# Kernel tuning notes

Hardware: AMD Instinct MI355X
Metric: run time of the kernel (lower is better)

Reference implementation:

```python
import jax, jax.numpy as jnp
import numpy as np

N, L, S, D, K, H, G = 512, 1024, 3, 128, 4, 32, 64


def setup_inputs() -> dict:
    key = jax.random.key(0)
    ks = jax.random.split(key, 12)
    f = lambda i, shape, s=1.0: jax.random.normal(ks[i], shape, dtype=jnp.float32) * s
    return dict(
        scores=f(0, (N, 1, L, S)),
        veh_repr=f(1, (N, 1, D)),
        cust_repr=f(2, (N, L, D)),
        edge_emb=f(3, (N, 1, L, D)),
        expert_w1=f(4, (K, S, H), 0.3),
        expert_b1=jnp.zeros((K, H), jnp.float32),
        expert_w2=f(5, (K, H, 1), 0.3),
        expert_b2=jnp.zeros((K, 1), jnp.float32),
        sit_w1=f(6, (2 * D, G), 0.05),
        sit_b1=jnp.zeros((G,), jnp.float32),
        sit_w2=f(7, (G, K), 0.1),
        sit_b2=jnp.zeros((K,), jnp.float32),
        cand_w=f(8, (S, K), 0.3),
        cand_b=jnp.zeros((K,), jnp.float32),
        edge_w=f(9, (D, K), 0.05),
        gate_balance=jnp.zeros((), jnp.float32),
    )


def reference(scores, veh_repr, cust_repr, edge_emb,
              expert_w1, expert_b1, expert_w2, expert_b2,
              sit_w1, sit_b1, sit_w2, sit_b2,
              cand_w, cand_b, edge_w, gate_balance):
    # Inference mode: no gate noise, no dropout (identity at eval).
    # Situation gating: vehicle repr + graph context -> (N,1,K) logits
    graph_ctx = cust_repr.mean(axis=1, keepdims=True)              # (N,1,D)
    sit_in = jnp.concatenate([veh_repr, graph_ctx], axis=-1)       # (N,1,2D)
    hg = jax.nn.gelu(sit_in @ sit_w1 + sit_b1, approximate=False)  # (N,1,G)
    sit_logits = hg @ sit_w2 + sit_b2                              # (N,1,K)

    # Candidate-level gating from raw scores + edge embeddings
    cand_logits = scores @ cand_w + cand_b + edge_emb @ edge_w     # (N,1,L,K)

    alpha = jax.nn.sigmoid(gate_balance)
    gate_logits = alpha * sit_logits[:, :, None, :] + (1.0 - alpha) * cand_logits
    gate_w = jax.nn.softmax(gate_logits, axis=-1)                  # (N,1,L,K)

    # Per-expert tiny MLP over the S score channels
    h = jax.nn.gelu(jnp.einsum('nqls,ksh->nqlkh', scores, expert_w1) + expert_b1,
                    approximate=False)                             # (N,1,L,K,H)
    expert_out = jnp.einsum('nqlkh,kho->nqlko', h, expert_w2)[..., 0] + expert_b2[:, 0]

    fused = (gate_w * expert_out).sum(axis=-1)                     # (N,1,L)
    return fused
```

## Files before the change

kernel.cpp:

```cpp
#include <hip/hip_runtime.h>

#define NN 512
#define LL 1024
#define SS 3
#define DD 128
#define KK 4
#define HH 32
#define GG 64

#define DPP_XOR1 0xB1
#define DPP_XOR2 0x4E
#define DPP_ROR4 0x124
#define DPP_ROR8 0x128
#define SWZ16 0x401F

template <int CTRL>
__device__ __forceinline__ float dppf(float x) {
    return __int_as_float(__builtin_amdgcn_update_dpp(
        0, __float_as_int(x), CTRL, 0xF, 0xF, true));
}
__device__ __forceinline__ float swz16f(float x) {
    return __int_as_float(__builtin_amdgcn_ds_swizzle(__float_as_int(x), SWZ16));
}

__device__ __forceinline__ float fast_gelu(float x) {
    const float c0 = 0.7978845608028654f;
    const float c1 = 0.7978845608028654f * 0.044715f;
    float u = x * x;
    float y = x * fmaf(c1, u, c0);
    float e = __expf(2.0f * y);
    float r = __builtin_amdgcn_rcpf(e + 1.0f);
    float t = fmaf(-2.0f, r, 1.0f);
    return 0.5f * x * (1.0f + t);
}

__global__ __launch_bounds__(512, 4) void k_all(
    const float* __restrict__ scores, const float* __restrict__ veh,
    const float* __restrict__ cust, const float* __restrict__ edge,
    const float* __restrict__ ew1, const float* __restrict__ eb1,
    const float* __restrict__ ew2, const float* __restrict__ eb2,
    const float* __restrict__ sw1, const float* __restrict__ sb1,
    const float* __restrict__ sw2, const float* __restrict__ sb2,
    const float* __restrict__ cand_w, const float* __restrict__ cand_b,
    const float* __restrict__ edge_w, const float* __restrict__ gbp,
    float* __restrict__ out)
{
    __shared__ float4 red[512];
    __shared__ float sin_[2 * DD];
    __shared__ float hg[GG];
    __shared__ float slds[KK];
    __shared__ float4 sc4[(LL * SS) / 4];

    const int n = blockIdx.x;
    const int t = threadIdx.x;
    const int lane = t & 63;
    const int r = lane & 31;

    const int ko = r & 3;
    const int jg = r >> 2;
    const bool kb0 = (r & 1) != 0;
    const bool kb1 = (r & 2) != 0;

    {
        const float4* sp4 = (const float4*)(scores + (size_t)n * LL * SS);
        sc4[t] = sp4[t];
        if (t < 256) sc4[512 + t] = sp4[512 + t];
    }

    const float4* ew4 = (const float4*)edge_w;
    const float4 wqa = ew4[4 * r + 0];
    const float4 wqb = ew4[4 * r + 1];
    const float4 wqc = ew4[4 * r + 2];
    const float4 wqd = ew4[4 * r + 3];
    const float cw0 = cand_w[0 * KK + ko];
    const float cw1 = cand_w[1 * KK + ko];
    const float cw2 = cand_w[2 * KK + ko];
    const float cb  = cand_b[ko];
    const float4* w1f = (const float4*)ew1;
    const float4 w1a = w1f[(ko * SS + 0) * (HH / 4) + jg];
    const float4 w1b = w1f[(ko * SS + 1) * (HH / 4) + jg];
    const float4 w1c = w1f[(ko * SS + 2) * (HH / 4) + jg];
    const float4 b1v = ((const float4*)eb1)[ko * (HH / 4) + jg];
    const float4 w2v = ((const float4*)ew2)[ko * (HH / 4) + jg];
    const float b2o8 = 0.125f * eb2[ko];
    const float gbv = gbp[0];
    const float alpha = 1.0f / (1.0f + __expf(-gbv));
    const float onema = 1.0f - alpha;

    const int c = t & 31;
    const int rs = t >> 5;
    const float4* cp = (const float4*)(cust + (size_t)n * LL * DD);
    float4 a0 = make_float4(0.f, 0.f, 0.f, 0.f), a1 = a0, a2 = a0, a3 = a0;
    #pragma unroll 4
    for (int i = 0; i < 16; ++i) {
        float4 v0 = cp[(rs + 16 * i      ) * 32 + c];
        float4 v1 = cp[(rs + 16 * i + 256) * 32 + c];
        float4 v2 = cp[(rs + 16 * i + 512) * 32 + c];
        float4 v3 = cp[(rs + 16 * i + 768) * 32 + c];
        a0.x += v0.x; a0.y += v0.y; a0.z += v0.z; a0.w += v0.w;
        a1.x += v1.x; a1.y += v1.y; a1.z += v1.z; a1.w += v1.w;
        a2.x += v2.x; a2.y += v2.y; a2.z += v2.z; a2.w += v2.w;
        a3.x += v3.x; a3.y += v3.y; a3.z += v3.z; a3.w += v3.w;
    }
    a0.x += a1.x + a2.x + a3.x;
    a0.y += a1.y + a2.y + a3.y;
    a0.z += a1.z + a2.z + a3.z;
    a0.w += a1.w + a2.w + a3.w;
    red[t] = a0;
    __syncthreads();

    if (t < 32) {
        float4 s = red[t];
        #pragma unroll
        for (int i = 1; i < 16; i++) {
            float4 v = red[i * 32 + t];
            s.x += v.x; s.y += v.y; s.z += v.z; s.w += v.w;
        }
        const float inv = 1.0f / (float)LL;
        sin_[DD + 4 * t + 0] = s.x * inv;
        sin_[DD + 4 * t + 1] = s.y * inv;
        sin_[DD + 4 * t + 2] = s.z * inv;
        sin_[DD + 4 * t + 3] = s.w * inv;
        float4 vv = ((const float4*)(veh + (size_t)n * DD))[t];
        sin_[4 * t + 0] = vv.x; sin_[4 * t + 1] = vv.y;
        sin_[4 * t + 2] = vv.z; sin_[4 * t + 3] = vv.w;
    }
    __syncthreads();

    float* redf = (float*)red;
    if (t < 256) {
        const int g = t & 63;
        const int part = t >> 6;
        float a = 0.f;
        #pragma unroll 8
        for (int i = 0; i < 64; ++i) {
            const int row = part * 64 + i;
            a = fmaf(sin_[row], sw1[row * GG + g], a);
        }
        redf[t] = a;
    }
    __syncthreads();
    if (t < GG) {
        float a = sb1[t] + redf[t] + redf[t + 64] + redf[t + 128] + redf[t + 192];
        hg[t] = fast_gelu(a);
    }
    __syncthreads();
    if (t < KK) {
        float a = sb2[t];
        #pragma unroll
        for (int g = 0; g < GG; g++)
            a = fmaf(hg[g], sw2[g * KK + t], a);
        slds[t] = a;
    }
    __syncthreads();

    const float sl0 = slds[0], sl1 = slds[1], sl2 = slds[2], sl3 = slds[3];
    float sa_ = kb0 ? sl1 : sl0;
    float sb_ = kb0 ? sl3 : sl2;
    float so  = kb1 ? sb_ : sa_;
    const float sbase = fmaf(alpha, so, onema * cb);

    const int base_el = t >> 5;
    const float* sc_lds = (const float*)sc4;
    const float* ed_base = edge + (size_t)n * LL * DD;
    float* out_base = out + (size_t)n * LL;

    for (int i = 0; i < 16; ++i) {
        const int e0 = base_el + i * 64;
        float4 ev[4];
        float s0[4], s1[4], s2[4];
        #pragma unroll
        for (int u = 0; u < 4; ++u)
            ev[u] = *(const float4*)(ed_base + (size_t)(e0 + u * 16) * DD + r * 4);
        #pragma unroll
        for (int u = 0; u < 4; ++u) {
            const int el = e0 + u * 16;
            s0[u] = sc_lds[el * 3 + 0];
            s1[u] = sc_lds[el * 3 + 1];
            s2[u] = sc_lds[el * 3 + 2];
        }

        float p0[4], p1[4], p2[4], p3[4];
        #pragma unroll
        for (int u = 0; u < 4; ++u) {
            p0[u] = fmaf(ev[u].x, wqa.x, fmaf(ev[u].y, wqb.x, fmaf(ev[u].z, wqc.x, ev[u].w * wqd.x)));
            p1[u] = fmaf(ev[u].x, wqa.y, fmaf(ev[u].y, wqb.y, fmaf(ev[u].z, wqc.y, ev[u].w * wqd.y)));
            p2[u] = fmaf(ev[u].x, wqa.z, fmaf(ev[u].y, wqb.z, fmaf(ev[u].z, wqc.z, ev[u].w * wqd.z)));
            p3[u] = fmaf(ev[u].x, wqa.w, fmaf(ev[u].y, wqb.w, fmaf(ev[u].z, wqc.w, ev[u].w * wqd.w)));
        }
        float P0[4], P2[4];
        #pragma unroll
        for (int u = 0; u < 4; ++u) {
            float g0 = kb0 ? p0[u] : p1[u];
            float g2 = kb0 ? p2[u] : p3[u];
            float k0 = kb0 ? p1[u] : p0[u];
            float k2 = kb0 ? p3[u] : p2[u];
            P0[u] = k0 + dppf<DPP_XOR1>(g0);
            P2[u] = k2 + dppf<DPP_XOR1>(g2);
        }
        float q[4];
        #pragma unroll
        for (int u = 0; u < 4; ++u) {
            float gv = kb1 ? P0[u] : P2[u];
            float kv = kb1 ? P2[u] : P0[u];
            q[u] = kv + dppf<DPP_XOR2>(gv);
        }
        #pragma unroll
        for (int u = 0; u < 4; ++u) q[u] += dppf<DPP_ROR4>(q[u]);
        #pragma unroll
        for (int u = 0; u < 4; ++u) q[u] += dppf<DPP_ROR8>(q[u]);
        #pragma unroll
        for (int u = 0; u < 4; ++u) q[u] += swz16f(q[u]);

        float ex[4];
        #pragma unroll
        for (int u = 0; u < 4; ++u) {
            float sdot = fmaf(s0[u], cw0, fmaf(s1[u], cw1, s2[u] * cw2));
            float gl = fmaf(onema, sdot + q[u], sbase);
            ex[u] = __expf(gl);
        }
        float se[4];
        #pragma unroll
        for (int u = 0; u < 4; ++u) se[u] = ex[u] + dppf<DPP_XOR1>(ex[u]);
        #pragma unroll
        for (int u = 0; u < 4; ++u) se[u] += dppf<DPP_XOR2>(se[u]);

        float tk[4];
        #pragma unroll
        for (int u = 0; u < 4; ++u) {
            float gw = ex[u] * __builtin_amdgcn_rcpf(se[u]);
            float z, h, acc;
            z = fmaf(s0[u], w1a.x, fmaf(s1[u], w1b.x, fmaf(s2[u], w1c.x, b1v.x))); h = fast_gelu(z); acc = h * w2v.x;
            z = fmaf(s0[u], w1a.y, fmaf(s1[u], w1b.y, fmaf(s2[u], w1c.y, b1v.y))); h = fast_gelu(z); acc = fmaf(h, w2v.y, acc);
            z = fmaf(s0[u], w1a.z, fmaf(s1[u], w1b.z, fmaf(s2[u], w1c.z, b1v.z))); h = fast_gelu(z); acc = fmaf(h, w2v.z, acc);
            z = fmaf(s0[u], w1a.w, fmaf(s1[u], w1b.w, fmaf(s2[u], w1c.w, b1v.w))); h = fast_gelu(z); acc = fmaf(h, w2v.w, acc);
            tk[u] = gw * (acc + b2o8);
        }
        #pragma unroll
        for (int u = 0; u < 4; ++u) tk[u] += dppf<DPP_XOR1>(tk[u]);
        #pragma unroll
        for (int u = 0; u < 4; ++u) tk[u] += dppf<DPP_XOR2>(tk[u]);
        #pragma unroll
        for (int u = 0; u < 4; ++u) tk[u] += dppf<DPP_ROR4>(tk[u]);
        #pragma unroll
        for (int u = 0; u < 4; ++u) tk[u] += dppf<DPP_ROR8>(tk[u]);
        #pragma unroll
        for (int u = 0; u < 4; ++u) tk[u] += swz16f(tk[u]);

        if (r == 0) {
            #pragma unroll
            for (int u = 0; u < 4; ++u)
                out_base[e0 + u * 16] = tk[u];
        }
    }
}

extern "C" void kernel_launch(void* const* d_in, const int* in_sizes, int n_in,
                              void* d_out, int out_size, void* d_ws, size_t ws_size,
                              hipStream_t stream)
{
    const float* scores = (const float*)d_in[0];
    const float* veh    = (const float*)d_in[1];
    const float* cust   = (const float*)d_in[2];
    const float* edge   = (const float*)d_in[3];
    const float* ew1    = (const float*)d_in[4];
    const float* eb1    = (const float*)d_in[5];
    const float* ew2    = (const float*)d_in[6];
    const float* eb2    = (const float*)d_in[7];
    const float* sw1    = (const float*)d_in[8];
    const float* sb1    = (const float*)d_in[9];
    const float* sw2    = (const float*)d_in[10];
    const float* sb2    = (const float*)d_in[11];
    const float* cw     = (const float*)d_in[12];
    const float* cb     = (const float*)d_in[13];
    const float* egw    = (const float*)d_in[14];
    const float* gb     = (const float*)d_in[15];
    float* out = (float*)d_out;

    hipLaunchKernelGGL(k_all, dim3(NN), dim3(512), 0, stream,
                       scores, veh, cust, edge, ew1, eb1, ew2, eb2,
                       sw1, sb1, sw2, sb2, cw, cb, egw, gb, out);
}
```

Baseline: 552.9 us.

## Fuse candidate gating into mean reduction via factored softmax with LDS staging

Moves the per-candidate edge-projection, expert MLP and exp computation into the same loop that sums cust_repr for the graph mean, so both large input streams are read in one pass. The softmax is factored into exp(alpha*situation logit) times exp(candidate logit), so the candidate-dependent part no longer waits for the situation MLP. Per-expert numerators and exponentials are staged in a 32 KB shared buffer and combined in a short final pass. This adds LDS pressure that may reduce occupancy, and drops the per-element softmax normalisation, which is less robust to large logits.

```diff
diff --git a/kernel.cpp b/kernel.cpp
--- a/kernel.cpp
+++ b/kernel.cpp
@@ -50,6 +50,7 @@
     __shared__ float hg[GG];
     __shared__ float slds[KK];
     __shared__ float4 sc4[(LL * SS) / 4];
+    __shared__ float elds[LL * 8];
 
     const int n = blockIdx.x;
     const int t = threadIdx.x;
@@ -86,22 +87,110 @@
     const float gbv = gbp[0];
     const float alpha = 1.0f / (1.0f + __expf(-gbv));
     const float onema = 1.0f - alpha;
+    const float cbase = onema * cb;
+
+    __syncthreads();
 
     const int c = t & 31;
     const int rs = t >> 5;
     const float4* cp = (const float4*)(cust + (size_t)n * LL * DD);
+    const int base_el = t >> 5;
+    const float* sc_lds = (const float*)sc4;
+    const float* ed_base = edge + (size_t)n * LL * DD;
+
     float4 a0 = make_float4(0.f, 0.f, 0.f, 0.f), a1 = a0, a2 = a0, a3 = a0;
-    #pragma unroll 4
+
     for (int i = 0; i < 16; ++i) {
+        const int e0 = base_el + i * 64;
+
+        float4 ev[4];
+        #pragma unroll
+        for (int u = 0; u < 4; ++u)
+            ev[u] = *(const float4*)(ed_base + (size_t)(e0 + u * 16) * DD + r * 4);
         float4 v0 = cp[(rs + 16 * i      ) * 32 + c];
         float4 v1 = cp[(rs + 16 * i + 256) * 32 + c];
         float4 v2 = cp[(rs + 16 * i + 512) * 32 + c];
         float4 v3 = cp[(rs + 16 * i + 768) * 32 + c];
+
+        float s0[4], s1[4], s2[4];
+        #pragma unroll
+        for (int u = 0; u < 4; ++u) {
+            const int el = e0 + u * 16;
+            s0[u] = sc_lds[el * 3 + 0];
+            s1[u] = sc_lds[el * 3 + 1];
+            s2[u] = sc_lds[el * 3 + 2];
+        }
+
+        float p0[4], p1[4], p2[4], p3[4];
+        #pragma unroll
+        for (int u = 0; u < 4; ++u) {
+            p0[u] = fmaf(ev[u].x, wqa.x, fmaf(ev[u].y, wqb.x, fmaf(ev[u].z, wqc.x, ev[u].w * wqd.x)));
+            p1[u] = fmaf(ev[u].x, wqa.y, fmaf(ev[u].y, wqb.y, fmaf(ev[u].z, wqc.y, ev[u].w * wqd.y)));
+            p2[u] = fmaf(ev[u].x, wqa.z, fmaf(ev[u].y, wqb.z, fmaf(ev[u].z, wqc.z, ev[u].w * wqd.z)));
+            p3[u] = fmaf(ev[u].x, wqa.w, fmaf(ev[u].y, wqb.w, fmaf(ev[u].z, wqc.w, ev[u].w * wqd.w)));
+        }
+        float P0[4], P2[4];
+        #pragma unroll
+        for (int u = 0; u < 4; ++u) {
+            float g0 = kb0 ? p0[u] : p1[u];
+            float g2 = kb0 ? p2[u] : p3[u];
+            float k0 = kb0 ? p1[u] : p0[u];
+            float k2 = kb0 ? p3[u] : p2[u];
+            P0[u] = k0 + dppf<DPP_XOR1>(g0);
+            P2[u] = k2 + dppf<DPP_XOR1>(g2);
+        }
+        float q[4];
+        #pragma unroll
+        for (int u = 0; u < 4; ++u) {
+            float gv = kb1 ? P0[u] : P2[u];
+            float kv = kb1 ? P2[u] : P0[u];
+            q[u] = kv + dppf<DPP_XOR2>(gv);
+        }
+        #pragma unroll
+        for (int u = 0; u < 4; ++u) q[u] += dppf<DPP_ROR4>(q[u]);
+        #pragma unroll
+        for (int u = 0; u < 4; ++u) q[u] += dppf<DPP_ROR8>(q[u]);
+        #pragma unroll
+        for (int u = 0; u < 4; ++u) q[u] += swz16f(q[u]);
+
+        float exc[4];
+        #pragma unroll
+        for (int u = 0; u < 4; ++u) {
+            float sdot = fmaf(s0[u], cw0, fmaf(s1[u], cw1, s2[u] * cw2));
+            exc[u] = __expf(fmaf(onema, sdot + q[u], cbase));
+        }
+
+        float vq[4];
+        #pragma unroll
+        for (int u = 0; u < 4; ++u) {
+            float z, h, acc;
+            z = fmaf(s0[u], w1a.x, fmaf(s1[u], w1b.x, fmaf(s2[u], w1c.x, b1v.x))); h = fast_gelu(z); acc = h * w2v.x;
+            z = fmaf(s0[u], w1a.y, fmaf(s1[u], w1b.y, fmaf(s2[u], w1c.y, b1v.y))); h = fast_gelu(z); acc = fmaf(h, w2v.y, acc);
+            z = fmaf(s0[u], w1a.z, fmaf(s1[u], w1b.z, fmaf(s2[u], w1c.z, b1v.z))); h = fast_gelu(z); acc = fmaf(h, w2v.z, acc);
+            z = fmaf(s0[u], w1a.w, fmaf(s1[u], w1b.w, fmaf(s2[u], w1c.w, b1v.w))); h = fast_gelu(z); acc = fmaf(h, w2v.w, acc);
+            vq[u] = exc[u] * (acc + b2o8);
+        }
+        #pragma unroll
+        for (int u = 0; u < 4; ++u) vq[u] += dppf<DPP_ROR4>(vq[u]);
+        #pragma unroll
+        for (int u = 0; u < 4; ++u) vq[u] += dppf<DPP_ROR8>(vq[u]);
+        #pragma unroll
+        for (int u = 0; u < 4; ++u) vq[u] += swz16f(vq[u]);
+
+        if (r < 8) {
+            #pragma unroll
+            for (int u = 0; u < 4; ++u) {
+                const int el = e0 + u * 16;
+                elds[el * 8 + r] = (r < 4) ? vq[u] : exc[u];
+            }
+        }
+
         a0.x += v0.x; a0.y += v0.y; a0.z += v0.z; a0.w += v0.w;
         a1.x += v1.x; a1.y += v1.y; a1.z += v1.z; a1.w += v1.w;
         a2.x += v2.x; a2.y += v2.y; a2.z += v2.z; a2.w += v2.w;
         a3.x += v3.x; a3.y += v3.y; a3.z += v3.z; a3.w += v3.w;
     }
+
     a0.x += a1.x + a2.x + a3.x;
     a0.y += a1.y + a2.y + a3.y;
     a0.z += a1.z + a2.z + a3.z;
@@ -154,104 +243,18 @@
     }
     __syncthreads();
 
-    const float sl0 = slds[0], sl1 = slds[1], sl2 = slds[2], sl3 = slds[3];
-    float sa_ = kb0 ? sl1 : sl0;
-    float sb_ = kb0 ? sl3 : sl2;
-    float so  = kb1 ? sb_ : sa_;
-    const float sbase = fmaf(alpha, so, onema * cb);
-
-    const int base_el = t >> 5;
-    const float* sc_lds = (const float*)sc4;
-    const float* ed_base = edge + (size_t)n * LL * DD;
+    const float m0 = __expf(alpha * slds[0]);
+    const float m1 = __expf(alpha * slds[1]);
+    const float m2 = __expf(alpha * slds[2]);
+    const float m3 = __expf(alpha * slds[3]);
     float* out_base = out + (size_t)n * LL;
-
-    for (int i = 0; i < 16; ++i) {
-        const int e0 = base_el + i * 64;
-        float4 ev[4];
-        float s0[4], s1[4], s2[4];
-        #pragma unroll
-        for (int u = 0; u < 4; ++u)
-            ev[u] = *(const float4*)(ed_base + (size_t)(e0 + u * 16) * DD + r * 4);
-        #pragma unroll
-        for (int u = 0; u < 4; ++u) {
-            const int el = e0 + u * 16;
-            s0[u] = sc_lds[el * 3 + 0];
-            s1[u] = sc_lds[el * 3 + 1];
-            s2[u] = sc_lds[el * 3 + 2];
-        }
-
-        float p0[4], p1[4], p2[4], p3[4];
-        #pragma unroll
-        for (int u = 0; u < 4; ++u) {
-            p0[u] = fmaf(ev[u].x, wqa.x, fmaf(ev[u].y, wqb.x, fmaf(ev[u].z, wqc.x, ev[u].w * wqd.x)));
-            p1[u] = fmaf(ev[u].x, wqa.y, fmaf(ev[u].y, wqb.y, fmaf(ev[u].z, wqc.y, ev[u].w * wqd.y)));
-            p2[u] = fmaf(ev[u].x, wqa.z, fmaf(ev[u].y, wqb.z, fmaf(ev[u].z, wqc.z, ev[u].w * wqd.z)));
-            p3[u] = fmaf(ev[u].x, wqa.w, fmaf(ev[u].y, wqb.w, fmaf(ev[u].z, wqc.w, ev[u].w * wqd.w)));
-        }
-        float P0[4], P2[4];
-        #pragma unroll
-        for (int u = 0; u < 4; ++u) {
-            float g0 = kb0 ? p0[u] : p1[u];
-            float g2 = kb0 ? p2[u] : p3[u];
-            float k0 = kb0 ? p1[u] : p0[u];
-            float k2 = kb0 ? p3[u] : p2[u];
-            P0[u] = k0 + dppf<DPP_XOR1>(g0);
-            P2[u] = k2 + dppf<DPP_XOR1>(g2);
-        }
-        float q[4];
-        #pragma unroll
-        for (int u = 0; u < 4; ++u) {
-            float gv = kb1 ? P0[u] : P2[u];
-            float kv = kb1 ? P2[u] : P0[u];
-            q[u] = kv + dppf<DPP_XOR2>(gv);
-        }
-        #pragma unroll
-        for (int u = 0; u < 4; ++u) q[u] += dppf<DPP_ROR4>(q[u]);
-        #pragma unroll
-        for (int u = 0; u < 4; ++u) q[u] += dppf<DPP_ROR8>(q[u]);
-        #pragma unroll
-        for (int u = 0; u < 4; ++u) q[u] += swz16f(q[u]);
-
-        float ex[4];
-        #pragma unroll
-        for (int u = 0; u < 4; ++u) {
-            float sdot = fmaf(s0[u], cw0, fmaf(s1[u], cw1, s2[u] * cw2));
-            float gl = fmaf(onema, sdot + q[u], sbase);
-            ex[u] = __expf(gl);
-        }
-        float se[4];
-        #pragma unroll
-        for (int u = 0; u < 4; ++u) se[u] = ex[u] + dppf<DPP_XOR1>(ex[u]);
-        #pragma unroll
-        for (int u = 0; u < 4; ++u) se[u] += dppf<DPP_XOR2>(se[u]);
-
-        float tk[4];
-        #pragma unroll
-        for (int u = 0; u < 4; ++u) {
-            float gw = ex[u] * __builtin_amdgcn_rcpf(se[u]);
-            float z, h, acc;
-            z = fmaf(s0[u], w1a.x, fmaf(s1[u], w1b.x, fmaf(s2[u], w1c.x, b1v.x))); h = fast_gelu(z); acc = h * w2v.x;
-            z = fmaf(s0[u], w1a.y, fmaf(s1[u], w1b.y, fmaf(s2[u], w1c.y, b1v.y))); h = fast_gelu(z); acc = fmaf(h, w2v.y, acc);
-            z = fmaf(s0[u], w1a.z, fmaf(s1[u], w1b.z, fmaf(s2[u], w1c.z, b1v.z))); h = fast_gelu(z); acc = fmaf(h, w2v.z, acc);
-            z = fmaf(s0[u], w1a.w, fmaf(s1[u], w1b.w, fmaf(s2[u], w1c.w, b1v.w))); h = fast_gelu(z); acc = fmaf(h, w2v.w, acc);
-            tk[u] = gw * (acc + b2o8);
-        }
-        #pragma unroll
-        for (int u = 0; u < 4; ++u) tk[u] += dppf<DPP_XOR1>(tk[u]);
-        #pragma unroll
-        for (int u = 0; u < 4; ++u) tk[u] += dppf<DPP_XOR2>(tk[u]);
-        #pragma unroll
-        for (int u = 0; u < 4; ++u) tk[u] += dppf<DPP_ROR4>(tk[u]);
-        #pragma unroll
-        for (int u = 0; u < 4; ++u) tk[u] += dppf<DPP_ROR8>(tk[u]);
-        #pragma unroll
-        for (int u = 0; u < 4; ++u) tk[u] += swz16f(tk[u]);
-
-        if (r == 0) {
-            #pragma unroll
-            for (int u = 0; u < 4; ++u)
-                out_base[e0 + u * 16] = tk[u];
-        }
+    #pragma unroll
+    for (int e = t; e < LL; e += 512) {
+        const float4 V = *(const float4*)&elds[e * 8];
+        const float4 E = *(const float4*)&elds[e * 8 + 4];
+        float num = fmaf(m0, V.x, fmaf(m1, V.y, fmaf(m2, V.z, m3 * V.w)));
+        float den = fmaf(m0, E.x, fmaf(m1, E.y, fmaf(m2, E.z, m3 * E.w)));
+        out_base[e] = num * __builtin_amdgcn_rcpf(den);
     }
 }
 
```

After: 537.5 us. -2.8%, faster.

## Split situation gating into separate kernel and parallelize element pass over chunks

Applied to the files above, without the earlier changes.

Moves the customer-mean and situation MLP into a first kernel that writes alpha-scaled situation logits per sample to the workspace. A second kernel handles the per-element gating and expert work across 8 chunks per sample in 256-thread blocks, processing one element per warp-half per iteration and prefetching the next edge row. It also reorganizes the softmax into one combined reduction of numerator and denominator, which drops one reduction stage. The goal is to remove the serial dependency of the element phase on the gating reduction within each block and to raise parallelism and occupancy. In exchange there is an extra kernel launch and a workspace round trip.

```diff
diff --git a/kernel.cpp b/kernel.cpp
--- a/kernel.cpp
+++ b/kernel.cpp
@@ -34,61 +34,21 @@
     return 0.5f * x * (1.0f + t);
 }
 
-__global__ __launch_bounds__(512, 4) void k_all(
-    const float* __restrict__ scores, const float* __restrict__ veh,
-    const float* __restrict__ cust, const float* __restrict__ edge,
-    const float* __restrict__ ew1, const float* __restrict__ eb1,
-    const float* __restrict__ ew2, const float* __restrict__ eb2,
+__global__ __launch_bounds__(512) void k_sit(
+    const float* __restrict__ veh, const float* __restrict__ cust,
     const float* __restrict__ sw1, const float* __restrict__ sb1,
     const float* __restrict__ sw2, const float* __restrict__ sb2,
-    const float* __restrict__ cand_w, const float* __restrict__ cand_b,
-    const float* __restrict__ edge_w, const float* __restrict__ gbp,
-    float* __restrict__ out)
+    const float* __restrict__ gbp, float* __restrict__ ws)
 {
     __shared__ float4 red[512];
     __shared__ float sin_[2 * DD];
     __shared__ float hg[GG];
-    __shared__ float slds[KK];
-    __shared__ float4 sc4[(LL * SS) / 4];
 
     const int n = blockIdx.x;
     const int t = threadIdx.x;
-    const int lane = t & 63;
-    const int r = lane & 31;
-
-    const int ko = r & 3;
-    const int jg = r >> 2;
-    const bool kb0 = (r & 1) != 0;
-    const bool kb1 = (r & 2) != 0;
-
-    {
-        const float4* sp4 = (const float4*)(scores + (size_t)n * LL * SS);
-        sc4[t] = sp4[t];
-        if (t < 256) sc4[512 + t] = sp4[512 + t];
-    }
-
-    const float4* ew4 = (const float4*)edge_w;
-    const float4 wqa = ew4[4 * r + 0];
-    const float4 wqb = ew4[4 * r + 1];
-    const float4 wqc = ew4[4 * r + 2];
-    const float4 wqd = ew4[4 * r + 3];
-    const float cw0 = cand_w[0 * KK + ko];
-    const float cw1 = cand_w[1 * KK + ko];
-    const float cw2 = cand_w[2 * KK + ko];
-    const float cb  = cand_b[ko];
-    const float4* w1f = (const float4*)ew1;
-    const float4 w1a = w1f[(ko * SS + 0) * (HH / 4) + jg];
-    const float4 w1b = w1f[(ko * SS + 1) * (HH / 4) + jg];
-    const float4 w1c = w1f[(ko * SS + 2) * (HH / 4) + jg];
-    const float4 b1v = ((const float4*)eb1)[ko * (HH / 4) + jg];
-    const float4 w2v = ((const float4*)ew2)[ko * (HH / 4) + jg];
-    const float b2o8 = 0.125f * eb2[ko];
-    const float gbv = gbp[0];
-    const float alpha = 1.0f / (1.0f + __expf(-gbv));
-    const float onema = 1.0f - alpha;
-
     const int c = t & 31;
     const int rs = t >> 5;
+
     const float4* cp = (const float4*)(cust + (size_t)n * LL * DD);
     float4 a0 = make_float4(0.f, 0.f, 0.f, 0.f), a1 = a0, a2 = a0, a3 = a0;
     #pragma unroll 4
@@ -150,108 +110,109 @@
         #pragma unroll
         for (int g = 0; g < GG; g++)
             a = fmaf(hg[g], sw2[g * KK + t], a);
-        slds[t] = a;
-    }
-    __syncthreads();
-
-    const float sl0 = slds[0], sl1 = slds[1], sl2 = slds[2], sl3 = slds[3];
-    float sa_ = kb0 ? sl1 : sl0;
-    float sb_ = kb0 ? sl3 : sl2;
-    float so  = kb1 ? sb_ : sa_;
-    const float sbase = fmaf(alpha, so, onema * cb);
-
-    const int base_el = t >> 5;
+        const float alpha = 1.0f / (1.0f + __expf(-gbp[0]));
+        ws[n * KK + t] = alpha * a;
+    }
+}
+
+__global__ __launch_bounds__(256, 6) void k_elem(
+    const float* __restrict__ scores, const float* __restrict__ edge,
+    const float* __restrict__ ew1, const float* __restrict__ eb1,
+    const float* __restrict__ ew2, const float* __restrict__ eb2,
+    const float* __restrict__ cand_w, const float* __restrict__ cand_b,
+    const float* __restrict__ edge_w, const float* __restrict__ gbp,
+    const float* __restrict__ ws, float* __restrict__ out)
+{
+    __shared__ float4 sc4[96];
+
+    const int b = blockIdx.x;
+    const int n = b >> 3;
+    const int chunk = b & 7;
+    const int t = threadIdx.x;
+    const int r = t & 31;
+    const int g = t >> 5;
+
+    {
+        const float4* sp4 = (const float4*)(scores + (size_t)n * LL * SS) + 96 * chunk;
+        if (t < 96) sc4[t] = sp4[t];
+    }
+
+    const int ko = r & 3;
+    const int jg = r >> 2;
+    const bool kb0 = (r & 1) != 0;
+    const bool kb1 = (r & 2) != 0;
+
+    const float4* ew4 = (const float4*)edge_w;
+    const float4 wqa = ew4[4 * r + 0];
+    const float4 wqb = ew4[4 * r + 1];
+    const float4 wqc = ew4[4 * r + 2];
+    const float4 wqd = ew4[4 * r + 3];
+    const float cw0 = cand_w[0 * KK + ko];
+    const float cw1 = cand_w[1 * KK + ko];
+    const float cw2 = cand_w[2 * KK + ko];
+    const float4* w1f = (const float4*)ew1;
+    const float4 w1a = w1f[(ko * SS + 0) * (HH / 4) + jg];
+    const float4 w1b = w1f[(ko * SS + 1) * (HH / 4) + jg];
+    const float4 w1c = w1f[(ko * SS + 2) * (HH / 4) + jg];
+    const float4 b1v = ((const float4*)eb1)[ko * (HH / 4) + jg];
+    const float4 w2v = ((const float4*)ew2)[ko * (HH / 4) + jg];
+    const float b2o8 = 0.125f * eb2[ko];
+    const float alpha = 1.0f / (1.0f + __expf(-gbp[0]));
+    const float onema = 1.0f - alpha;
+    const float eb_ = fmaf(onema, cand_b[ko], ws[n * KK + ko]);
+
+    __syncthreads();
+
     const float* sc_lds = (const float*)sc4;
-    const float* ed_base = edge + (size_t)n * LL * DD;
-    float* out_base = out + (size_t)n * LL;
+    const float* ed_base = edge + (size_t)n * LL * DD + (size_t)(chunk * 128) * DD;
+    float* outp = out + (size_t)n * LL + chunk * 128;
+
+    float4 ev = *(const float4*)(ed_base + (size_t)g * DD + r * 4);
 
     for (int i = 0; i < 16; ++i) {
-        const int e0 = base_el + i * 64;
-        float4 ev[4];
-        float s0[4], s1[4], s2[4];
-        #pragma unroll
-        for (int u = 0; u < 4; ++u)
-            ev[u] = *(const float4*)(ed_base + (size_t)(e0 + u * 16) * DD + r * 4);
-        #pragma unroll
-        for (int u = 0; u < 4; ++u) {
-            const int el = e0 + u * 16;
-            s0[u] = sc_lds[el * 3 + 0];
-            s1[u] = sc_lds[el * 3 + 1];
-            s2[u] = sc_lds[el * 3 + 2];
-        }
-
-        float p0[4], p1[4], p2[4], p3[4];
-        #pragma unroll
-        for (int u = 0; u < 4; ++u) {
-            p0[u] = fmaf(ev[u].x, wqa.x, fmaf(ev[u].y, wqb.x, fmaf(ev[u].z, wqc.x, ev[u].w * wqd.x)));
-            p1[u] = fmaf(ev[u].x, wqa.y, fmaf(ev[u].y, wqb.y, fmaf(ev[u].z, wqc.y, ev[u].w * wqd.y)));
-            p2[u] = fmaf(ev[u].x, wqa.z, fmaf(ev[u].y, wqb.z, fmaf(ev[u].z, wqc.z, ev[u].w * wqd.z)));
-            p3[u] = fmaf(ev[u].x, wqa.w, fmaf(ev[u].y, wqb.w, fmaf(ev[u].z, wqc.w, ev[u].w * wqd.w)));
-        }
-        float P0[4], P2[4];
-        #pragma unroll
-        for (int u = 0; u < 4; ++u) {
-            float g0 = kb0 ? p0[u] : p1[u];
-            float g2 = kb0 ? p2[u] : p3[u];
-            float k0 = kb0 ? p1[u] : p0[u];
-            float k2 = kb0 ? p3[u] : p2[u];
-            P0[u] = k0 + dppf<DPP_XOR1>(g0);
-            P2[u] = k2 + dppf<DPP_XOR1>(g2);
-        }
-        float q[4];
-        #pragma unroll
-        for (int u = 0; u < 4; ++u) {
-            float gv = kb1 ? P0[u] : P2[u];
-            float kv = kb1 ? P2[u] : P0[u];
-            q[u] = kv + dppf<DPP_XOR2>(gv);
-        }
-        #pragma unroll
-        for (int u = 0; u < 4; ++u) q[u] += dppf<DPP_ROR4>(q[u]);
-        #pragma unroll
-        for (int u = 0; u < 4; ++u) q[u] += dppf<DPP_ROR8>(q[u]);
-        #pragma unroll
-        for (int u = 0; u < 4; ++u) q[u] += swz16f(q[u]);
-
-        float ex[4];
-        #pragma unroll
-        for (int u = 0; u < 4; ++u) {
-            float sdot = fmaf(s0[u], cw0, fmaf(s1[u], cw1, s2[u] * cw2));
-            float gl = fmaf(onema, sdot + q[u], sbase);
-            ex[u] = __expf(gl);
-        }
-        float se[4];
-        #pragma unroll
-        for (int u = 0; u < 4; ++u) se[u] = ex[u] + dppf<DPP_XOR1>(ex[u]);
-        #pragma unroll
-        for (int u = 0; u < 4; ++u) se[u] += dppf<DPP_XOR2>(se[u]);
-
-        float tk[4];
-        #pragma unroll
-        for (int u = 0; u < 4; ++u) {
-            float gw = ex[u] * __builtin_amdgcn_rcpf(se[u]);
-            float z, h, acc;
-            z = fmaf(s0[u], w1a.x, fmaf(s1[u], w1b.x, fmaf(s2[u], w1c.x, b1v.x))); h = fast_gelu(z); acc = h * w2v.x;
-            z = fmaf(s0[u], w1a.y, fmaf(s1[u], w1b.y, fmaf(s2[u], w1c.y, b1v.y))); h = fast_gelu(z); acc = fmaf(h, w2v.y, acc);
-            z = fmaf(s0[u], w1a.z, fmaf(s1[u], w1b.z, fmaf(s2[u], w1c.z, b1v.z))); h = fast_gelu(z); acc = fmaf(h, w2v.z, acc);
-            z = fmaf(s0[u], w1a.w, fmaf(s1[u], w1b.w, fmaf(s2[u], w1c.w, b1v.w))); h = fast_gelu(z); acc = fmaf(h, w2v.w, acc);
-            tk[u] = gw * (acc + b2o8);
-        }
-        #pragma unroll
-        for (int u = 0; u < 4; ++u) tk[u] += dppf<DPP_XOR1>(tk[u]);
-        #pragma unroll
-        for (int u = 0; u < 4; ++u) tk[u] += dppf<DPP_XOR2>(tk[u]);
-        #pragma unroll
-        for (int u = 0; u < 4; ++u) tk[u] += dppf<DPP_ROR4>(tk[u]);
-        #pragma unroll
-        for (int u = 0; u < 4; ++u) tk[u] += dppf<DPP_ROR8>(tk[u]);
-        #pragma unroll
-        for (int u = 0; u < 4; ++u) tk[u] += swz16f(tk[u]);
-
-        if (r == 0) {
-            #pragma unroll
-            for (int u = 0; u < 4; ++u)
-                out_base[e0 + u * 16] = tk[u];
-        }
+        const int le = i * 8 + g;
+        const int ln = (i < 15) ? le + 8 : le;
+        float4 evn = *(const float4*)(ed_base + (size_t)ln * DD + r * 4);
+
+        const float s0 = sc_lds[le * 3 + 0];
+        const float s1 = sc_lds[le * 3 + 1];
+        const float s2 = sc_lds[le * 3 + 2];
+
+        float p0 = fmaf(ev.x, wqa.x, fmaf(ev.y, wqb.x, fmaf(ev.z, wqc.x, ev.w * wqd.x)));
+        float p1 = fmaf(ev.x, wqa.y, fmaf(ev.y, wqb.y, fmaf(ev.z, wqc.y, ev.w * wqd.y)));
+        float p2 = fmaf(ev.x, wqa.z, fmaf(ev.y, wqb.z, fmaf(ev.z, wqc.z, ev.w * wqd.z)));
+        float p3 = fmaf(ev.x, wqa.w, fmaf(ev.y, wqb.w, fmaf(ev.z, wqc.w, ev.w * wqd.w)));
+
+        float g0 = kb0 ? p0 : p1, k0 = kb0 ? p1 : p0;
+        float g2 = kb0 ? p2 : p3, k2 = kb0 ? p3 : p2;
+        float P0 = k0 + dppf<DPP_XOR1>(g0);
+        float P2 = k2 + dppf<DPP_XOR1>(g2);
+        float gv = kb1 ? P0 : P2, kv = kb1 ? P2 : P0;
+        float q = kv + dppf<DPP_XOR2>(gv);
+        q += dppf<DPP_ROR4>(q);
+        q += dppf<DPP_ROR8>(q);
+        q += swz16f(q);
+
+        const float sdot = fmaf(s0, cw0, fmaf(s1, cw1, s2 * cw2));
+        const float excm = __expf(fmaf(onema, sdot + q, eb_));
+
+        float z, h, acc;
+        z = fmaf(s0, w1a.x, fmaf(s1, w1b.x, fmaf(s2, w1c.x, b1v.x))); h = fast_gelu(z); acc = h * w2v.x;
+        z = fmaf(s0, w1a.y, fmaf(s1, w1b.y, fmaf(s2, w1c.y, b1v.y))); h = fast_gelu(z); acc = fmaf(h, w2v.y, acc);
+        z = fmaf(s0, w1a.z, fmaf(s1, w1b.z, fmaf(s2, w1c.z, b1v.z))); h = fast_gelu(z); acc = fmaf(h, w2v.z, acc);
+        z = fmaf(s0, w1a.w, fmaf(s1, w1b.w, fmaf(s2, w1c.w, b1v.w))); h = fast_gelu(z); acc = fmaf(h, w2v.w, acc);
+        float vq = excm * (acc + b2o8);
+
+        float de = excm;
+        vq += dppf<DPP_XOR1>(vq);  de += dppf<DPP_XOR1>(de);
+        vq += dppf<DPP_XOR2>(vq);  de += dppf<DPP_XOR2>(de);
+        vq += dppf<DPP_ROR4>(vq);  de += dppf<DPP_ROR4>(de);
+        vq += dppf<DPP_ROR8>(vq);  de += dppf<DPP_ROR8>(de);
+        vq += swz16f(vq);          de += swz16f(de);
+
+        if (r == 0) outp[le] = 8.0f * vq * __builtin_amdgcn_rcpf(de);
+
+        ev = evn;
     }
 }
 
@@ -276,8 +237,11 @@
     const float* egw    = (const float*)d_in[14];
     const float* gb     = (const float*)d_in[15];
     float* out = (float*)d_out;
-
-    hipLaunchKernelGGL(k_all, dim3(NN), dim3(512), 0, stream,
-                       scores, veh, cust, edge, ew1, eb1, ew2, eb2,
-                       sw1, sb1, sw2, sb2, cw, cb, egw, gb, out);
-}
+    float* ws  = (float*)d_ws;
+
+    hipLaunchKernelGGL(k_sit, dim3(NN), dim3(512), 0, stream,
+                       veh, cust, sw1, sb1, sw2, sb2, gb, ws);
+    hipLaunchKernelGGL(k_elem, dim3(NN * 8), dim3(256), 0, stream,
+                       scores, edge, ew1, eb1, ew2, eb2,
+                       cw, cb, egw, gb, ws, out);
+}
```

Result: no change. 548.4 us (-0.8%).
